# Kernel optimization log

Hardware: AMD Instinct MI355X
Metric: run time of the kernel (lower is better)

The kernel has to match this reference:

```python
import jax, jax.numpy as jnp
import numpy as np

BLANK = 0
SIZE_AVERAGE = True


def rnnt_loss(acts, labels, act_lens, label_lens):
    # acts: (B, T, U+1, V) raw logits; warp-transducer applies log_softmax internally
    B, T, U1, V = acts.shape
    U = U1 - 1
    logp = jax.nn.log_softmax(acts, axis=-1)          # (B,T,U1,V)
    lp_blank = logp[..., BLANK]                       # (B,T,U1)
    # emission log-prob of label u at grid point (t,u): logp[b,t,u,labels[b,u]]
    lp_emit = jnp.take_along_axis(
        logp[:, :, :U, :], labels[:, None, :, None].astype(jnp.int32), axis=3
    )[..., 0]                                         # (B,T,U)

    # alpha[0,0]=0 ; alpha[0,u] = sum_{k<u} emit[0,k]
    row0 = jnp.concatenate(
        [jnp.zeros((B, 1), acts.dtype), jnp.cumsum(lp_emit[:, 0, :], axis=1)], axis=1
    )                                                 # (B,U1)

    def outer(prev_row, xs):
        blank_prev, emit_t = xs                       # (B,U1), (B,U)
        fb = prev_row + blank_prev                    # arrive via blank from t-1
        def inner(carry, x):
            fb_u, em_prev = x                         # (B,), (B,)
            a = jnp.logaddexp(fb_u, carry + em_prev)  # blank vs emit path
            return a, a
        _, rest = jax.lax.scan(inner, fb[:, 0], (fb[:, 1:].T, emit_t.T))  # (U,B)
        row = jnp.concatenate([fb[:, :1], rest.T], axis=1)               # (B,U1)
        return row, row

    xs = (jnp.moveaxis(lp_blank[:, :-1, :], 1, 0),   # (T-1,B,U1)
          jnp.moveaxis(lp_emit[:, 1:, :], 1, 0))     # (T-1,B,U)
    _, rows = jax.lax.scan(outer, row0, xs)          # (T-1,B,U1)
    alpha = jnp.concatenate([row0[None], rows], axis=0)  # (T,B,U1)

    b_idx = jnp.arange(B)
    t_idx = act_lens.astype(jnp.int32) - 1
    u_idx = label_lens.astype(jnp.int32)
    loglike = alpha[t_idx, b_idx, u_idx] + lp_blank[b_idx, t_idx, u_idx]
    total = -jnp.sum(loglike)
    if SIZE_AVERAGE:
        total = total / B
    return total.reshape(1)


def setup_inputs() -> dict:
    key = jax.random.key(0)
    k1, k2, k3, k4 = jax.random.split(key, 4)
    B, T, U, V = 8, 256, 100, 128
    acts = jax.random.normal(k1, (B, T, U + 1, V), dtype=jnp.float32)
    labels = jax.random.randint(k2, (B, U), 0, V, dtype=jnp.int64)
    act_lens = jax.random.randint(k3, (B,), T // 2, T + 1, dtype=jnp.int32)
    label_lens = jax.random.randint(k4, (B,), U // 2, U + 1, dtype=jnp.int32)
    return {"acts": acts, "labels": labels, "act_lens": act_lens, "label_lens": label_lens}


def reference(acts, labels, act_lens, label_lens):
    return rnnt_loss(acts, labels, act_lens, label_lens)
```

## Files before the change

kernel.cpp:

```cpp
#include <hip/hip_runtime.h>
#include <math.h>

#define B_DIM  8
#define T_DIM  256
#define U_DIM  100
#define U1_DIM 101
#define V_DIM  128

#define ROWU   128
#define DROWS  360
#define NV     352
#define VROWS  418
#define VROWB  1280
#define PL     416
#define DEPTH  16
#define NEGF   (-8.0e29f)
#define FILLP  0xF122F122u
#define LOG2E  1.4426950408889634f
#define LN2    0.69314718055994530942f

typedef unsigned uv2 __attribute__((ext_vector_type(2)));

__device__ __forceinline__ float ubit(unsigned u) { return __builtin_bit_cast(float, u); }

__device__ __forceinline__ float logadd2(float a, float b) {
    float m = fmaxf(a, b);
    float e = exp2f(-fabsf(a - b));
    return m + log2f(1.0f + e);
}
__device__ __forceinline__ float lse3(float a, float b, float c) {
    float m = fmaxf(fmaxf(a, b), c);
    float s = exp2f(a - m) + exp2f(b - m) + exp2f(c - m);
    return m + log2f(s);
}
__device__ __forceinline__ float lse5(float a, float b, float c, float d, float e) {
    float m = fmaxf(fmaxf(fmaxf(a, b), c), fmaxf(d, e));
    float s = exp2f(a - m) + exp2f(b - m) + exp2f(c - m) + exp2f(d - m) + exp2f(e - m);
    return m + log2f(s);
}

__device__ __forceinline__ float lane_shr1(float x) {
    int r = __builtin_amdgcn_update_dpp(0, __builtin_bit_cast(int, x),
                                        0x138 , 0xF, 0xF, true);
    return __builtin_bit_cast(float, r);
}

__device__ __forceinline__ unsigned f2bf(float f) {
    unsigned u = __builtin_bit_cast(unsigned, f);
    u += 0x7FFF + ((u >> 16) & 1);
    return u >> 16;
}

struct W2 { float tA, mA, lA, tB, mB, lB; };
__device__ __forceinline__ W2 buildW2(uv2 c0 , uv2 cm , int l) {
    float BL0a = ubit(c0.x << 16), EM0a = ubit(c0.x & 0xFFFF0000u);
    float BL0b = ubit(c0.y << 16), EM0b = ubit(c0.y & 0xFFFF0000u);
    float BLma = ubit(cm.x << 16), EMma = ubit(cm.x & 0xFFFF0000u);
    float BLmb = ubit(cm.y << 16), EMmb = ubit(cm.y & 0xFFFF0000u);
    float BLmp = lane_shr1(BLmb), EMmp = lane_shr1(EMmb);
    W2 w;
    w.tA = BLma + BL0a;
    w.mA = logadd2(EMma + BL0a, BLmp + EM0a);
    w.lA = EMmp + EM0a;
    w.tB = BLmb + BL0b;
    w.mB = logadd2(EMmb + BL0b, BLma + EM0b);
    w.lB = EMma + EM0b;
    if (l == 0) { w.mA = NEGF; w.lA = NEGF; w.lB = NEGF; }
    return w;
}

__global__ __launch_bounds__(256) void fill_kernel(uint4* __restrict__ p, int n4,
                                                   int* __restrict__ counter) {
    int i = blockIdx.x * 256 + threadIdx.x;
    if (i < n4) p[i] = make_uint4(FILLP, FILLP, FILLP, FILLP);
    if (i == 0) *counter = 0;
}

__global__ __launch_bounds__(256) void lsm_kernel(
    const float* __restrict__ acts, const int* __restrict__ labels,
    const int* __restrict__ act_lens, const int* __restrict__ label_lens,
    unsigned short* __restrict__ comb, int nrows)
{
    int rid = blockIdx.x * 8 + (threadIdx.x >> 5);
    if (rid >= nrows) return;
    int hl = threadIdx.x & 31;

    int u  = rid % U1_DIM;
    int bt = rid / U1_DIM;
    int b  = bt / T_DIM;
    int t  = bt - b * T_DIM;
    if (t >= act_lens[b] || u > label_lens[b]) return;

    const float* row = acts + (size_t)rid * V_DIM;
    float4 x = *reinterpret_cast<const float4*>(row + 4 * hl);
    float4 y = make_float4(x.x * LOG2E, x.y * LOG2E, x.z * LOG2E, x.w * LOG2E);

    float s = exp2f(y.x) + exp2f(y.y) + exp2f(y.z) + exp2f(y.w);
    #pragma unroll
    for (int off = 16; off; off >>= 1) s += __shfl_xor(s, off);
    float lse2 = log2f(s);

    unsigned short* C = comb + (size_t)b * DROWS * (ROWU * 2);
    int d = t + u + 1;

    if (hl == 0)
        C[(size_t)d * (ROWU * 2) + 2 * u] = (unsigned short)f2bf(y.x - lse2);
    if (u < U_DIM) {
        int lab = labels[b * U_DIM + u];
        if (hl == (lab >> 2)) {
            int r = lab & 3;
            float v = (r == 0) ? y.x : (r == 1) ? y.y : (r == 2) ? y.z : y.w;
            C[(size_t)d * (ROWU * 2) + 2 * u + 3] = (unsigned short)f2bf(v - lse2);
        }
    }
}

__global__ __launch_bounds__(256) void v_kernel(
    const unsigned* __restrict__ comb, unsigned* __restrict__ V)
{
    int wid = blockIdx.x * 4 + (threadIdx.x >> 6);
    if (wid >= B_DIM * NV) return;
    int l  = threadIdx.x & 63;
    int b  = wid / NV;
    int ri = wid - b * NV;
    int dt = ri + 4;

    const unsigned* C = comb + ((size_t)b * DROWS + dt) * ROWU + 2 * l;
    uv2 c0 = *(const uv2*)(C);
    uv2 c1 = *(const uv2*)(C - ROWU);
    uv2 c2 = *(const uv2*)(C - 2 * ROWU);
    uv2 c3 = *(const uv2*)(C - 3 * ROWU);

    W2 P = buildW2(c0, c1, l);
    W2 Q = buildW2(c2, c3, l);

    float Qt_b1 = lane_shr1(Q.tB), Qm_b1 = lane_shr1(Q.mB), Ql_b1 = lane_shr1(Q.lB);
    float Qt_a1 = lane_shr1(Q.tA), Qm_a1 = lane_shr1(Q.mA), Ql_a1 = lane_shr1(Q.lA);

    float V0a = P.tA + Q.tA;
    float V1a = logadd2(P.tA + Q.mA, P.mA + Qt_b1);
    float V2a = lse3(P.tA + Q.lA, P.mA + Qm_b1, P.lA + Qt_a1);
    float V3a = logadd2(P.mA + Ql_b1, P.lA + Qm_a1);
    float V4a = P.lA + Ql_a1;
    float V0b = P.tB + Q.tB;
    float V1b = logadd2(P.tB + Q.mB, P.mB + Q.tA);
    float V2b = lse3(P.tB + Q.lB, P.mB + Q.mA, P.lB + Qt_b1);
    float V3b = logadd2(P.mB + Q.lA, P.lB + Qm_b1);
    float V4b = P.lB + Ql_b1;

    if (l == 0) { V1a = NEGF; V2a = NEGF; V3a = NEGF; V4a = NEGF; }

    if (l < 52) {
        char* row = (char*)V + ((size_t)b * VROWS + ri) * VROWB + 8 * l;
        uv2 p0, p1, p2;
        p0.x = f2bf(V0a) | (f2bf(V1a) << 16);  p0.y = f2bf(V0b) | (f2bf(V1b) << 16);
        p1.x = f2bf(V2a) | (f2bf(V3a) << 16);  p1.y = f2bf(V2b) | (f2bf(V3b) << 16);
        p2.x = f2bf(V4a);                      p2.y = f2bf(V4b);
        *(uv2*)(row)          = p0;
        *(uv2*)(row + PL)     = p1;
        *(uv2*)(row + 2 * PL) = p2;
    }
}

__global__ __launch_bounds__(64, 1) void dp_kernel(
    const unsigned* __restrict__ comb, const unsigned* __restrict__ V,
    const int* __restrict__ act_lens, const int* __restrict__ label_lens,
    float* __restrict__ loglike, int* __restrict__ counter,
    float* __restrict__ out)
{
    const int b = blockIdx.x;
    const int l = threadIdx.x;
    const int tl    = act_lens[b] - 1;
    const int ul    = label_lens[b];
    const int dfin  = tl + ul;
    const int start = dfin & 3;
    const int niter = dfin >> 2;

    const unsigned* combB = comb + (size_t)b * DROWS * ROWU;
    const char* Vb = (const char*)V + (size_t)b * VROWS * VROWB + 8 * l;

    unsigned fbu = combB[(size_t)(dfin + 1) * ROWU + ul];
    float fin_bl = ubit(fbu << 16);

    float v0 = (l == 0) ? 0.0f : NEGF;
    float v1 = NEGF;
    for (int d = 1; d <= start; ++d) {
        uv2 c = *(const uv2*)(combB + (size_t)d * ROWU + 2 * l);
        float bl0 = ubit(c.x << 16), em0 = ubit(c.x & 0xFFFF0000u);
        float bl1 = ubit(c.y << 16), em1 = ubit(c.y & 0xFFFF0000u);
        float left0 = lane_shr1(v1);
        float a0 = v0 + bl0, p0 = left0 + em0;
        float a1 = v1 + bl1, p1 = v0 + em1;
        v0 = logadd2(a0, p0);
        v1 = logadd2(a1, p1);
    }
    float rf0 = NEGF, rf1 = NEGF;

    asm volatile("s_waitcnt vmcnt(0)" ::: "memory");

    uv2 r0[DEPTH], r1[DEPTH], r2[DEPTH];
    #pragma unroll
    for (int j = 0; j < DEPTH; ++j) {
        int rr = start + 4 * j; rr = rr < VROWS - 2 ? rr : VROWS - 3;
        const char* p = Vb + (size_t)rr * VROWB;
        asm volatile("global_load_dwordx2 %0, %1, off" : "=v"(r0[j]) : "v"(p));
        asm volatile("global_load_dwordx2 %0, %1, off" : "=v"(r1[j]) : "v"(p + PL));
        asm volatile("global_load_dwordx2 %0, %1, off" : "=v"(r2[j]) : "v"(p + 2 * PL));
    }

    const int ngroups = (niter + DEPTH - 1) / DEPTH;
    for (int g = 0; g < ngroups; ++g) {
        const int it0 = g * DEPTH;
        #pragma unroll
        for (int q = 0; q < 4; ++q) {
            asm volatile("s_waitcnt vmcnt(36)");
            __builtin_amdgcn_sched_barrier(0);
            #pragma unroll
            for (int j4 = 0; j4 < 4; ++j4) {
                const int J = q * 4 + j4;
                const int it = it0 + J;
                uv2 a0 = r0[J], a1 = r1[J], a2 = r2[J];
                float V0a = ubit(a0.x << 16), V1a = ubit(a0.x & 0xFFFF0000u);
                float V0b = ubit(a0.y << 16), V1b = ubit(a0.y & 0xFFFF0000u);
                float V2a = ubit(a1.x << 16), V3a = ubit(a1.x & 0xFFFF0000u);
                float V2b = ubit(a1.y << 16), V3b = ubit(a1.y & 0xFFFF0000u);
                float V4a = ubit(a2.x << 16), V4b = ubit(a2.y << 16);
                float s1 = lane_shr1(v1);
                float s0 = lane_shr1(v0);
                float s3 = lane_shr1(s1);
                float s2 = lane_shr1(s0);
                float nA = lse5(v0 + V0a, s1 + V1a, s0 + V2a, s3 + V3a, s2 + V4a);
                float nB = lse5(v1 + V0b, v0 + V1b, s1 + V2b, s0 + V3b, s3 + V4b);
                if (it == niter - 1) { rf0 = nA; rf1 = nB; }
                v0 = nA; v1 = nB;
                int rr = start + 4 * (it + DEPTH); rr = rr < VROWS - 2 ? rr : VROWS - 3;
                const char* p = Vb + (size_t)rr * VROWB;
                asm volatile("global_load_dwordx2 %0, %1, off" : "=v"(r0[J]) : "v"(p));
                asm volatile("global_load_dwordx2 %0, %1, off" : "=v"(r1[J]) : "v"(p + PL));
                asm volatile("global_load_dwordx2 %0, %1, off" : "=v"(r2[J]) : "v"(p + 2 * PL));
            }
        }
    }

    float res = (ul & 1) ? rf1 : rf0;
    if (l == (ul >> 1)) {
        loglike[b] = LN2 * (res + fin_bl);
        __threadfence();
        int old = atomicAdd(counter, 1);
        if (old == B_DIM - 1) {
            __threadfence();
            float s = 0.0f;
            #pragma unroll
            for (int i = 0; i < B_DIM; ++i)
                s += __hip_atomic_load(&loglike[i], __ATOMIC_RELAXED,
                                       __HIP_MEMORY_SCOPE_AGENT);
            out[0] = -s / (float)B_DIM;
        }
    }
}

extern "C" void kernel_launch(void* const* d_in, const int* in_sizes, int n_in,
                              void* d_out, int out_size, void* d_ws, size_t ws_size,
                              hipStream_t stream) {
    const float* acts       = (const float*)d_in[0];
    const int*   labels     = (const int*)d_in[1];
    const int*   act_lens   = (const int*)d_in[2];
    const int*   label_lens = (const int*)d_in[3];

    unsigned* comb    = (unsigned*)d_ws;
    unsigned* V       = comb + (size_t)B_DIM * DROWS * ROWU;
    float*    loglike = (float*)((char*)V + (size_t)B_DIM * VROWS * VROWB);
    int*      counter = (int*)(loglike + B_DIM);

    int nrows   = B_DIM * T_DIM * U1_DIM;
    int nblocks = (nrows + 7) / 8;

    int nfill4  = (B_DIM * DROWS * ROWU) / 4;
    fill_kernel<<<(nfill4 + 255) / 256, 256, 0, stream>>>((uint4*)comb, nfill4, counter);
    lsm_kernel<<<nblocks, 256, 0, stream>>>(acts, labels, act_lens, label_lens,
                                            (unsigned short*)comb, nrows);
    int vwaves = B_DIM * NV;
    v_kernel<<<(vwaves + 3) / 4, 256, 0, stream>>>(comb, V);
    dp_kernel<<<B_DIM, 64, 0, stream>>>(comb, V, act_lens, label_lens,
                                        loglike, counter, (float*)d_out);
}
```

Baseline: 56.91 us.

## Fuse V precompute into DP kernel via LDS and drop fill kernel

Removes the fill and separate V-building kernels. The DP kernel now uses 8 waves per batch to build the 4-step transition table into shared memory, synchronizes, then one wave runs the recurrence reading from LDS. The fill is replaced by explicit validity masking of out-of-range grid entries, and the counter is reset in the lsm kernel and after use. This cuts two launches and global round trips, but the table build now sits serially before the recurrence inside only 8 blocks, and a host attribute call is added each launch.

```diff
diff --git a/kernel.cpp b/kernel.cpp
--- a/kernel.cpp
+++ b/kernel.cpp
@@ -9,15 +9,13 @@
 
 #define ROWU   128
 #define DROWS  360
-#define NV     352
-#define VROWS  418
-#define VROWB  1280
-#define PL     416
-#define DEPTH  16
 #define NEGF   (-8.0e29f)
-#define FILLP  0xF122F122u
 #define LOG2E  1.4426950408889634f
 #define LN2    0.69314718055994530942f
+
+#define VROWU  312
+#define NITMAX 88
+#define LDS_BYTES (NITMAX * VROWU * 4)
 
 typedef unsigned uv2 __attribute__((ext_vector_type(2)));
 
@@ -51,12 +49,62 @@
     return u >> 16;
 }
 
+__global__ __launch_bounds__(256) void lsm_kernel(
+    const float* __restrict__ acts, const int* __restrict__ labels,
+    const int* __restrict__ act_lens, const int* __restrict__ label_lens,
+    unsigned short* __restrict__ comb, int* __restrict__ counter, int nrows)
+{
+    if (blockIdx.x == 0 && threadIdx.x == 0) *counter = 0;
+
+    int rid = blockIdx.x * 8 + (threadIdx.x >> 5);
+    if (rid >= nrows) return;
+    int hl = threadIdx.x & 31;
+
+    int u  = rid % U1_DIM;
+    int bt = rid / U1_DIM;
+    int b  = bt / T_DIM;
+    int t  = bt - b * T_DIM;
+    if (t >= act_lens[b] || u > label_lens[b]) return;
+
+    const float* row = acts + (size_t)rid * V_DIM;
+    float4 x = *reinterpret_cast<const float4*>(row + 4 * hl);
+    float4 y = make_float4(x.x * LOG2E, x.y * LOG2E, x.z * LOG2E, x.w * LOG2E);
+
+    float s = exp2f(y.x) + exp2f(y.y) + exp2f(y.z) + exp2f(y.w);
+    #pragma unroll
+    for (int off = 16; off; off >>= 1) s += __shfl_xor(s, off);
+    float lse2 = log2f(s);
+
+    unsigned short* C = comb + (size_t)b * DROWS * (ROWU * 2);
+    int d = t + u + 1;
+
+    if (hl == 0)
+        C[(size_t)d * (ROWU * 2) + 2 * u] = (unsigned short)f2bf(y.x - lse2);
+    if (u < U_DIM) {
+        int lab = labels[b * U_DIM + u];
+        if (hl == (lab >> 2)) {
+            int r = lab & 3;
+            float v = (r == 0) ? y.x : (r == 1) ? y.y : (r == 2) ? y.z : y.w;
+            C[(size_t)d * (ROWU * 2) + 2 * u + 3] = (unsigned short)f2bf(v - lse2);
+        }
+    }
+}
+
 struct W2 { float tA, mA, lA, tB, mB, lB; };
-__device__ __forceinline__ W2 buildW2(uv2 c0 , uv2 cm , int l) {
+__device__ __forceinline__ W2 buildW2m(uv2 c0, uv2 cm, int l, int d, int tl, int ul) {
+    const int ua = 2 * l, ub = 2 * l + 1;
     float BL0a = ubit(c0.x << 16), EM0a = ubit(c0.x & 0xFFFF0000u);
     float BL0b = ubit(c0.y << 16), EM0b = ubit(c0.y & 0xFFFF0000u);
     float BLma = ubit(cm.x << 16), EMma = ubit(cm.x & 0xFFFF0000u);
     float BLmb = ubit(cm.y << 16), EMmb = ubit(cm.y & 0xFFFF0000u);
+    BL0a = (ua <= ul && (unsigned)(d - 1 - ua) <= (unsigned)tl) ? BL0a : NEGF;
+    BL0b = (ub <= ul && (unsigned)(d - 1 - ub) <= (unsigned)tl) ? BL0b : NEGF;
+    EM0a = (ua >= 1 && ua <= ul && (unsigned)(d - ua) <= (unsigned)tl) ? EM0a : NEGF;
+    EM0b = (ub <= ul && (unsigned)(d - ub) <= (unsigned)tl) ? EM0b : NEGF;
+    BLma = (ua <= ul && (unsigned)(d - 2 - ua) <= (unsigned)tl) ? BLma : NEGF;
+    BLmb = (ub <= ul && (unsigned)(d - 1 - ub) <= (unsigned)tl) ? BLmb : NEGF;
+    EMma = (ua >= 1 && ua <= ul && (unsigned)(d - 1 - ua) <= (unsigned)tl) ? EMma : NEGF;
+    EMmb = (ub <= ul && (unsigned)(d - 1 - ub) <= (unsigned)tl) ? EMmb : NEGF;
     float BLmp = lane_shr1(BLmb), EMmp = lane_shr1(EMmb);
     W2 w;
     w.tA = BLma + BL0a;
@@ -69,107 +117,17 @@
     return w;
 }
 
-__global__ __launch_bounds__(256) void fill_kernel(uint4* __restrict__ p, int n4,
-                                                   int* __restrict__ counter) {
-    int i = blockIdx.x * 256 + threadIdx.x;
-    if (i < n4) p[i] = make_uint4(FILLP, FILLP, FILLP, FILLP);
-    if (i == 0) *counter = 0;
-}
-
-__global__ __launch_bounds__(256) void lsm_kernel(
-    const float* __restrict__ acts, const int* __restrict__ labels,
-    const int* __restrict__ act_lens, const int* __restrict__ label_lens,
-    unsigned short* __restrict__ comb, int nrows)
-{
-    int rid = blockIdx.x * 8 + (threadIdx.x >> 5);
-    if (rid >= nrows) return;
-    int hl = threadIdx.x & 31;
-
-    int u  = rid % U1_DIM;
-    int bt = rid / U1_DIM;
-    int b  = bt / T_DIM;
-    int t  = bt - b * T_DIM;
-    if (t >= act_lens[b] || u > label_lens[b]) return;
-
-    const float* row = acts + (size_t)rid * V_DIM;
-    float4 x = *reinterpret_cast<const float4*>(row + 4 * hl);
-    float4 y = make_float4(x.x * LOG2E, x.y * LOG2E, x.z * LOG2E, x.w * LOG2E);
-
-    float s = exp2f(y.x) + exp2f(y.y) + exp2f(y.z) + exp2f(y.w);
-    #pragma unroll
-    for (int off = 16; off; off >>= 1) s += __shfl_xor(s, off);
-    float lse2 = log2f(s);
-
-    unsigned short* C = comb + (size_t)b * DROWS * (ROWU * 2);
-    int d = t + u + 1;
-
-    if (hl == 0)
-        C[(size_t)d * (ROWU * 2) + 2 * u] = (unsigned short)f2bf(y.x - lse2);
-    if (u < U_DIM) {
-        int lab = labels[b * U_DIM + u];
-        if (hl == (lab >> 2)) {
-            int r = lab & 3;
-            float v = (r == 0) ? y.x : (r == 1) ? y.y : (r == 2) ? y.z : y.w;
-            C[(size_t)d * (ROWU * 2) + 2 * u + 3] = (unsigned short)f2bf(v - lse2);
-        }
-    }
-}
-
-__global__ __launch_bounds__(256) void v_kernel(
-    const unsigned* __restrict__ comb, unsigned* __restrict__ V)
-{
-    int wid = blockIdx.x * 4 + (threadIdx.x >> 6);
-    if (wid >= B_DIM * NV) return;
-    int l  = threadIdx.x & 63;
-    int b  = wid / NV;
-    int ri = wid - b * NV;
-    int dt = ri + 4;
-
-    const unsigned* C = comb + ((size_t)b * DROWS + dt) * ROWU + 2 * l;
-    uv2 c0 = *(const uv2*)(C);
-    uv2 c1 = *(const uv2*)(C - ROWU);
-    uv2 c2 = *(const uv2*)(C - 2 * ROWU);
-    uv2 c3 = *(const uv2*)(C - 3 * ROWU);
-
-    W2 P = buildW2(c0, c1, l);
-    W2 Q = buildW2(c2, c3, l);
-
-    float Qt_b1 = lane_shr1(Q.tB), Qm_b1 = lane_shr1(Q.mB), Ql_b1 = lane_shr1(Q.lB);
-    float Qt_a1 = lane_shr1(Q.tA), Qm_a1 = lane_shr1(Q.mA), Ql_a1 = lane_shr1(Q.lA);
-
-    float V0a = P.tA + Q.tA;
-    float V1a = logadd2(P.tA + Q.mA, P.mA + Qt_b1);
-    float V2a = lse3(P.tA + Q.lA, P.mA + Qm_b1, P.lA + Qt_a1);
-    float V3a = logadd2(P.mA + Ql_b1, P.lA + Qm_a1);
-    float V4a = P.lA + Ql_a1;
-    float V0b = P.tB + Q.tB;
-    float V1b = logadd2(P.tB + Q.mB, P.mB + Q.tA);
-    float V2b = lse3(P.tB + Q.lB, P.mB + Q.mA, P.lB + Qt_b1);
-    float V3b = logadd2(P.mB + Q.lA, P.lB + Qm_b1);
-    float V4b = P.lB + Ql_b1;
-
-    if (l == 0) { V1a = NEGF; V2a = NEGF; V3a = NEGF; V4a = NEGF; }
-
-    if (l < 52) {
-        char* row = (char*)V + ((size_t)b * VROWS + ri) * VROWB + 8 * l;
-        uv2 p0, p1, p2;
-        p0.x = f2bf(V0a) | (f2bf(V1a) << 16);  p0.y = f2bf(V0b) | (f2bf(V1b) << 16);
-        p1.x = f2bf(V2a) | (f2bf(V3a) << 16);  p1.y = f2bf(V2b) | (f2bf(V3b) << 16);
-        p2.x = f2bf(V4a);                      p2.y = f2bf(V4b);
-        *(uv2*)(row)          = p0;
-        *(uv2*)(row + PL)     = p1;
-        *(uv2*)(row + 2 * PL) = p2;
-    }
-}
-
-__global__ __launch_bounds__(64, 1) void dp_kernel(
-    const unsigned* __restrict__ comb, const unsigned* __restrict__ V,
+__global__ __launch_bounds__(512, 1) void dp_kernel(
+    const unsigned* __restrict__ comb,
     const int* __restrict__ act_lens, const int* __restrict__ label_lens,
     float* __restrict__ loglike, int* __restrict__ counter,
     float* __restrict__ out)
 {
+    extern __shared__ unsigned sV[];
+
     const int b = blockIdx.x;
-    const int l = threadIdx.x;
+    const int l = threadIdx.x & 63;
+    const int w = threadIdx.x >> 6;
     const int tl    = act_lens[b] - 1;
     const int ul    = label_lens[b];
     const int dfin  = tl + ul;
@@ -177,72 +135,87 @@
     const int niter = dfin >> 2;
 
     const unsigned* combB = comb + (size_t)b * DROWS * ROWU;
-    const char* Vb = (const char*)V + (size_t)b * VROWS * VROWB + 8 * l;
-
-    unsigned fbu = combB[(size_t)(dfin + 1) * ROWU + ul];
-    float fin_bl = ubit(fbu << 16);
+
+    for (int it = w; it < niter; it += 8) {
+        const int dt = start + 4 * (it + 1);
+        const unsigned* C = combB + (size_t)dt * ROWU + 2 * l;
+        uv2 c0 = *(const uv2*)(C);
+        uv2 c1 = *(const uv2*)(C - ROWU);
+        uv2 c2 = *(const uv2*)(C - 2 * ROWU);
+        uv2 c3 = *(const uv2*)(C - 3 * ROWU);
+
+        W2 P = buildW2m(c0, c1, l, dt,     tl, ul);
+        W2 Q = buildW2m(c2, c3, l, dt - 2, tl, ul);
+
+        float Qt_b1 = lane_shr1(Q.tB), Qm_b1 = lane_shr1(Q.mB), Ql_b1 = lane_shr1(Q.lB);
+        float Qt_a1 = lane_shr1(Q.tA), Qm_a1 = lane_shr1(Q.mA), Ql_a1 = lane_shr1(Q.lA);
+
+        float V0a = P.tA + Q.tA;
+        float V1a = logadd2(P.tA + Q.mA, P.mA + Qt_b1);
+        float V2a = lse3(P.tA + Q.lA, P.mA + Qm_b1, P.lA + Qt_a1);
+        float V3a = logadd2(P.mA + Ql_b1, P.lA + Qm_a1);
+        float V4a = P.lA + Ql_a1;
+        float V0b = P.tB + Q.tB;
+        float V1b = logadd2(P.tB + Q.mB, P.mB + Q.tA);
+        float V2b = lse3(P.tB + Q.lB, P.mB + Q.mA, P.lB + Qt_b1);
+        float V3b = logadd2(P.mB + Q.lA, P.lB + Qm_b1);
+        float V4b = P.lB + Ql_b1;
+        if (l == 0) { V1a = NEGF; V2a = NEGF; V3a = NEGF; V4a = NEGF; }
+
+        if (l < 52) {
+            unsigned* ro = sV + it * VROWU;
+            ro[2 * l]           = f2bf(V0a) | (f2bf(V1a) << 16);
+            ro[2 * l + 1]       = f2bf(V0b) | (f2bf(V1b) << 16);
+            ro[104 + 2 * l]     = f2bf(V2a) | (f2bf(V3a) << 16);
+            ro[104 + 2 * l + 1] = f2bf(V2b) | (f2bf(V3b) << 16);
+            ro[208 + 2 * l]     = f2bf(V4a);
+            ro[208 + 2 * l + 1] = f2bf(V4b);
+        }
+    }
+    __syncthreads();
+    if (w != 0) return;
+
+    float fin_bl = ubit(combB[(size_t)(dfin + 1) * ROWU + ul] << 16);
 
     float v0 = (l == 0) ? 0.0f : NEGF;
     float v1 = NEGF;
     for (int d = 1; d <= start; ++d) {
         uv2 c = *(const uv2*)(combB + (size_t)d * ROWU + 2 * l);
+        const int ua = 2 * l, ub = 2 * l + 1;
         float bl0 = ubit(c.x << 16), em0 = ubit(c.x & 0xFFFF0000u);
         float bl1 = ubit(c.y << 16), em1 = ubit(c.y & 0xFFFF0000u);
+        bl0 = (ua <= ul && (unsigned)(d - 1 - ua) <= (unsigned)tl) ? bl0 : NEGF;
+        bl1 = (ub <= ul && (unsigned)(d - 1 - ub) <= (unsigned)tl) ? bl1 : NEGF;
+        em0 = (ua >= 1 && ua <= ul && (unsigned)(d - ua) <= (unsigned)tl) ? em0 : NEGF;
+        em1 = (ub <= ul && (unsigned)(d - ub) <= (unsigned)tl) ? em1 : NEGF;
         float left0 = lane_shr1(v1);
         float a0 = v0 + bl0, p0 = left0 + em0;
         float a1 = v1 + bl1, p1 = v0 + em1;
         v0 = logadd2(a0, p0);
         v1 = logadd2(a1, p1);
     }
-    float rf0 = NEGF, rf1 = NEGF;
-
-    asm volatile("s_waitcnt vmcnt(0)" ::: "memory");
-
-    uv2 r0[DEPTH], r1[DEPTH], r2[DEPTH];
-    #pragma unroll
-    for (int j = 0; j < DEPTH; ++j) {
-        int rr = start + 4 * j; rr = rr < VROWS - 2 ? rr : VROWS - 3;
-        const char* p = Vb + (size_t)rr * VROWB;
-        asm volatile("global_load_dwordx2 %0, %1, off" : "=v"(r0[j]) : "v"(p));
-        asm volatile("global_load_dwordx2 %0, %1, off" : "=v"(r1[j]) : "v"(p + PL));
-        asm volatile("global_load_dwordx2 %0, %1, off" : "=v"(r2[j]) : "v"(p + 2 * PL));
-    }
-
-    const int ngroups = (niter + DEPTH - 1) / DEPTH;
-    for (int g = 0; g < ngroups; ++g) {
-        const int it0 = g * DEPTH;
-        #pragma unroll
-        for (int q = 0; q < 4; ++q) {
-            asm volatile("s_waitcnt vmcnt(36)");
-            __builtin_amdgcn_sched_barrier(0);
-            #pragma unroll
-            for (int j4 = 0; j4 < 4; ++j4) {
-                const int J = q * 4 + j4;
-                const int it = it0 + J;
-                uv2 a0 = r0[J], a1 = r1[J], a2 = r2[J];
-                float V0a = ubit(a0.x << 16), V1a = ubit(a0.x & 0xFFFF0000u);
-                float V0b = ubit(a0.y << 16), V1b = ubit(a0.y & 0xFFFF0000u);
-                float V2a = ubit(a1.x << 16), V3a = ubit(a1.x & 0xFFFF0000u);
-                float V2b = ubit(a1.y << 16), V3b = ubit(a1.y & 0xFFFF0000u);
-                float V4a = ubit(a2.x << 16), V4b = ubit(a2.y << 16);
-                float s1 = lane_shr1(v1);
-                float s0 = lane_shr1(v0);
-                float s3 = lane_shr1(s1);
-                float s2 = lane_shr1(s0);
-                float nA = lse5(v0 + V0a, s1 + V1a, s0 + V2a, s3 + V3a, s2 + V4a);
-                float nB = lse5(v1 + V0b, v0 + V1b, s1 + V2b, s0 + V3b, s3 + V4b);
-                if (it == niter - 1) { rf0 = nA; rf1 = nB; }
-                v0 = nA; v1 = nB;
-                int rr = start + 4 * (it + DEPTH); rr = rr < VROWS - 2 ? rr : VROWS - 3;
-                const char* p = Vb + (size_t)rr * VROWB;
-                asm volatile("global_load_dwordx2 %0, %1, off" : "=v"(r0[J]) : "v"(p));
-                asm volatile("global_load_dwordx2 %0, %1, off" : "=v"(r1[J]) : "v"(p + PL));
-                asm volatile("global_load_dwordx2 %0, %1, off" : "=v"(r2[J]) : "v"(p + 2 * PL));
-            }
-        }
-    }
-
-    float res = (ul & 1) ? rf1 : rf0;
+
+    #pragma unroll 4
+    for (int it = 0; it < niter; ++it) {
+        const unsigned* ro = sV + it * VROWU;
+        uv2 a0 = *(const uv2*)(ro + 2 * l);
+        uv2 a1 = *(const uv2*)(ro + 104 + 2 * l);
+        uv2 a2 = *(const uv2*)(ro + 208 + 2 * l);
+        float V0a = ubit(a0.x << 16), V1a = ubit(a0.x & 0xFFFF0000u);
+        float V0b = ubit(a0.y << 16), V1b = ubit(a0.y & 0xFFFF0000u);
+        float V2a = ubit(a1.x << 16), V3a = ubit(a1.x & 0xFFFF0000u);
+        float V2b = ubit(a1.y << 16), V3b = ubit(a1.y & 0xFFFF0000u);
+        float V4a = ubit(a2.x << 16), V4b = ubit(a2.y << 16);
+        float s1 = lane_shr1(v1);
+        float s0 = lane_shr1(v0);
+        float s3 = lane_shr1(s1);
+        float s2 = lane_shr1(s0);
+        float nA = lse5(v0 + V0a, s1 + V1a, s0 + V2a, s3 + V3a, s2 + V4a);
+        float nB = lse5(v1 + V0b, v0 + V1b, s1 + V2b, s0 + V3b, s3 + V4b);
+        v0 = nA; v1 = nB;
+    }
+
+    float res = (ul & 1) ? v1 : v0;
     if (l == (ul >> 1)) {
         loglike[b] = LN2 * (res + fin_bl);
         __threadfence();
@@ -255,6 +228,8 @@
                 s += __hip_atomic_load(&loglike[i], __ATOMIC_RELAXED,
                                        __HIP_MEMORY_SCOPE_AGENT);
             out[0] = -s / (float)B_DIM;
+            __hip_atomic_store(counter, 0, __ATOMIC_RELAXED,
+                               __HIP_MEMORY_SCOPE_AGENT);
         }
     }
 }
@@ -268,19 +243,17 @@
     const int*   label_lens = (const int*)d_in[3];
 
     unsigned* comb    = (unsigned*)d_ws;
-    unsigned* V       = comb + (size_t)B_DIM * DROWS * ROWU;
-    float*    loglike = (float*)((char*)V + (size_t)B_DIM * VROWS * VROWB);
+    float*    loglike = (float*)(comb + (size_t)B_DIM * DROWS * ROWU);
     int*      counter = (int*)(loglike + B_DIM);
 
     int nrows   = B_DIM * T_DIM * U1_DIM;
     int nblocks = (nrows + 7) / 8;
 
-    int nfill4  = (B_DIM * DROWS * ROWU) / 4;
-    fill_kernel<<<(nfill4 + 255) / 256, 256, 0, stream>>>((uint4*)comb, nfill4, counter);
+    hipFuncSetAttribute(reinterpret_cast<const void*>(dp_kernel),
+                        hipFuncAttributeMaxDynamicSharedMemorySize, LDS_BYTES);
+
     lsm_kernel<<<nblocks, 256, 0, stream>>>(acts, labels, act_lens, label_lens,
-                                            (unsigned short*)comb, nrows);
-    int vwaves = B_DIM * NV;
-    v_kernel<<<(vwaves + 3) / 4, 256, 0, stream>>>(comb, V);
-    dp_kernel<<<B_DIM, 64, 0, stream>>>(comb, V, act_lens, label_lens,
-                                        loglike, counter, (float*)d_out);
-}
+                                            (unsigned short*)comb, counter, nrows);
+    dp_kernel<<<B_DIM, 512, LDS_BYTES, stream>>>(comb, act_lens, label_lens,
+                                                 loglike, counter, (float*)d_out);
+}
```

Measured after the change: 59.51 us. 4.6% more time.
